# Kernel optimization log

Measured on AMD Instinct MI355X. Metric: run time of the kernel, lower is better.

## Reference

```python
import jax, jax.numpy as jnp
import numpy as np

NODE_LEN = 200000; E = 1000000; BATCH = 128; NT = 2048
IN_FEATS = 256; HID = 128; L1 = 13; L2 = 30; NHEAD = 8; GAMMA = 0.1


def _type_att(xs, W, b, q):
    # xs: [N, T, d] -> [N, d]; type-level (semantic) attention
    s = jnp.einsum('ntd,d->nt', jnp.tanh(xs @ W + b), q)
    a = jax.nn.softmax(s, axis=1)
    return jnp.einsum('nt,ntd->nd', a, xs)


def _add_att(qv, kv, Wq, Wk, v):
    # qv: [N, d], kv: [N, L, d] -> [N, d]; additive attention over L
    t = jnp.tanh((qv @ Wq)[:, None, :] + kv @ Wk)
    a = jax.nn.softmax(jnp.einsum('nld,d->nl', t, v), axis=1)
    return jnp.einsum('nl,nld->nd', a, kv)


def _mha(h, W, b):
    # h: [N, L, D]; W: [4, D, D] (q,k,v,o); b: [4, D]
    N, L, D = h.shape
    hd = D // NHEAD
    def proj(i):
        return (h @ W[i] + b[i]).reshape(N, L, NHEAD, hd).transpose(0, 2, 1, 3)
    q, k, v = proj(0), proj(1), proj(2)
    a = jax.nn.softmax(jnp.einsum('nhld,nhmd->nhlm', q, k) / jnp.sqrt(jnp.float32(hd)), axis=-1)
    o = jnp.einsum('nhlm,nhmd->nhld', a, v).transpose(0, 2, 1, 3).reshape(N, L, D)
    return o @ W[3] + b[3]


def _forward(x, edge_index, batch, rootindex, type_x0, type_x1, type_x2, root1, parent1,
             root2, parent2, type_x3, root3, type_x4, root4, adj,
             W1, b1, W2, b2, mha_W, mha_b, att_Wq, att_Wk, att_v, fuse_W, fuse_b,
             gat_W, gat_a_src, gat_a_dst, ta_W, ta_b, ta_q, gc2_W, gc2_b, fin_W, fin_b):
    n = x.shape[0]
    loop = jnp.arange(n, dtype=edge_index.dtype)
    row = jnp.concatenate([edge_index[0], loop])
    col = jnp.concatenate([edge_index[1], loop])
    deg = jax.ops.segment_sum(jnp.ones(row.shape[0], x.dtype), col, num_segments=n)
    dinv = jax.lax.rsqrt(jnp.maximum(deg, 1.0))
    norm = (dinv[row] * dinv[col])[:, None]

    def gcn(h, W, b):
        m = (h @ W)[row] * norm
        return jax.ops.segment_sum(m, col, num_segments=n) + b

    h1 = gcn(x, W1, b1)                          # conv1
    root_extend = h1[rootindex[batch]]           # per-graph root broadcast (replaces python loop)
    h = jax.nn.relu(jnp.concatenate([h1, root_extend], axis=1))
    h2 = jax.nn.relu(gcn(h, W2, b2))             # conv2
    # sentinel zero row == eye(node_len+1, node_len) one-hot gather semantics
    hp = jnp.concatenate([h2, jnp.zeros((1, h2.shape[1]), h2.dtype)], axis=0)

    x0 = [hp[type_x0]]
    for i, (tx, rid, pid) in enumerate([(type_x1, root1, parent1), (type_x2, root2, parent2)]):
        lst, rt, pr = hp[tx], hp[rid], hp[pid]
        ids = jnp.stack([pr, rt], axis=1)        # [N, 2, d]
        att = _add_att(lst, ids, att_Wq[i], att_Wk[i], att_v[i])
        alpha = jax.nn.sigmoid(jnp.concatenate([lst, att], axis=-1) @ fuse_W[i] + fuse_b[i])[:, None]
        x0.append(alpha * lst + (1.0 - alpha) * att)
    for i, (tx, rid) in enumerate([(type_x3, root3), (type_x4, root4)]):
        seq = _mha(hp[tx], mha_W[i], mha_b[i])   # [N, L, d]
        rt = hp[rid]
        att = _add_att(rt, seq, att_Wq[2 + i], att_Wk[2 + i], att_v[2 + i])
        alpha = jax.nn.sigmoid(jnp.concatenate([rt, att], axis=-1) @ fuse_W[2 + i] + fuse_b[2 + i])[:, None]
        x0.append(alpha * rt + (1.0 - alpha) * att)
    x0.append(hp[type_x0])

    # heterogeneous graph attention conv (gc1) + per-type attention fusion (at1)
    H = jnp.stack([x0[t] @ gat_W[t] for t in range(6)])  # [6, NT, d]
    mask = adj > 0
    x1 = []
    for t1 in range(6):
        msgs = []
        for t2 in range(6):
            e = (H[t1] @ gat_a_src[t1, t2])[:, None] + (H[t2] @ gat_a_dst[t1, t2])[None, :]
            s = jnp.where(mask[t1, t2], jax.nn.leaky_relu(e, negative_slope=GAMMA), -1e9)
            msgs.append(jax.nn.softmax(s, axis=1) @ H[t2])
        m = jnp.stack(msgs, axis=1)                      # [NT, 6, d]
        x1.append(jax.nn.relu(_type_att(m, ta_W[t1], ta_b[t1], ta_q[t1])))
    X1 = jnp.stack(x1)                                   # [6, NT, d]

    # second hop: dense GraphConvolution (gc2) + at2; only type 5 feeds the head
    hx = X1 @ gc2_W
    msgs5 = jnp.einsum('snm,smd->snd', adj[5], hx) + gc2_b
    x2_5 = _type_att(msgs5.transpose(1, 0, 2), ta_W[11], ta_b[11], ta_q[11])
    return jax.nn.log_softmax(x2_5 @ fin_W + fin_b, axis=-1)


def setup_inputs() -> dict:
    key = jax.random.key(0)
    ks = jax.random.split(key, 32)
    f32 = jnp.float32
    x = jax.random.normal(ks[0], (NODE_LEN, IN_FEATS), f32)
    edge_index = jax.random.randint(ks[1], (2, E), 0, NODE_LEN, dtype=jnp.int32)
    batch = jax.random.randint(ks[2], (NODE_LEN,), 0, BATCH, dtype=jnp.int32)
    rootindex = jax.random.randint(ks[3], (BATCH,), 0, NODE_LEN, dtype=jnp.int32)
    idx = lambda k, shape: jax.random.randint(k, shape, 0, NODE_LEN, dtype=jnp.int32)
    type_x0 = idx(ks[4], (NT,)); type_x1 = idx(ks[5], (NT,)); type_x2 = idx(ks[6], (NT,))
    root1 = idx(ks[7], (NT,)); parent1 = idx(ks[8], (NT,))
    root2 = idx(ks[9], (NT,)); parent2 = idx(ks[10], (NT,))
    type_x3 = idx(ks[11], (NT, L1)); root3 = idx(ks[12], (NT,))
    type_x4 = idx(ks[13], (NT, L2)); root4 = idx(ks[14], (NT,))
    adj = (jax.random.uniform(ks[15], (6, 6, NT, NT)) < 0.02).astype(f32)
    p = lambda k, shape: 0.02 * jax.random.normal(k, shape, f32)
    W1 = p(ks[16], (IN_FEATS, HID)); b1 = jnp.zeros((HID,), f32)
    W2 = p(ks[17], (2 * HID, HID)); b2 = jnp.zeros((HID,), f32)
    mha_W = p(ks[18], (2, 4, HID, HID)); mha_b = jnp.zeros((2, 4, HID), f32)
    att_Wq = p(ks[19], (4, HID, HID)); att_Wk = p(ks[20], (4, HID, HID)); att_v = p(ks[21], (4, HID))
    fuse_W = p(ks[22], (4, 2 * HID)); fuse_b = jnp.zeros((4,), f32)
    gat_W = p(ks[23], (6, HID, HID)); gat_a_src = p(ks[24], (6, 6, HID)); gat_a_dst = p(ks[25], (6, 6, HID))
    ta_W = p(ks[26], (12, HID, HID)); ta_b = jnp.zeros((12, HID), f32); ta_q = p(ks[27], (12, HID))
    gc2_W = p(ks[28], (HID, HID)); gc2_b = jnp.zeros((HID,), f32)
    fin_W = p(ks[29], (HID, 4)); fin_b = jnp.zeros((4,), f32)
    return dict(x=x, edge_index=edge_index, batch=batch, rootindex=rootindex,
                type_x0=type_x0, type_x1=type_x1, type_x2=type_x2,
                root1=root1, parent1=parent1, root2=root2, parent2=parent2,
                type_x3=type_x3, root3=root3, type_x4=type_x4, root4=root4, adj=adj,
                W1=W1, b1=b1, W2=W2, b2=b2, mha_W=mha_W, mha_b=mha_b,
                att_Wq=att_Wq, att_Wk=att_Wk, att_v=att_v, fuse_W=fuse_W, fuse_b=fuse_b,
                gat_W=gat_W, gat_a_src=gat_a_src, gat_a_dst=gat_a_dst,
                ta_W=ta_W, ta_b=ta_b, ta_q=ta_q, gc2_W=gc2_W, gc2_b=gc2_b,
                fin_W=fin_W, fin_b=fin_b)


def reference(x, edge_index, batch, rootindex, type_x0, type_x1, type_x2, root1, parent1,
              root2, parent2, type_x3, root3, type_x4, root4, adj,
              W1, b1, W2, b2, mha_W, mha_b, att_Wq, att_Wk, att_v, fuse_W, fuse_b,
              gat_W, gat_a_src, gat_a_dst, ta_W, ta_b, ta_q, gc2_W, gc2_b, fin_W, fin_b):
    return _forward(x, edge_index, batch, rootindex, type_x0, type_x1, type_x2, root1, parent1,
                    root2, parent2, type_x3, root3, type_x4, root4, adj,
                    W1, b1, W2, b2, mha_W, mha_b, att_Wq, att_Wk, att_v, fuse_W, fuse_b,
                    gat_W, gat_a_src, gat_a_dst, ta_W, ta_b, ta_q, gc2_W, gc2_b, fin_W, fin_b)
```

## Files before the change

### kernel.cpp

```cpp
#include <hip/hip_runtime.h>
#include <hip/hip_bf16.h>
#include <math.h>


typedef unsigned short u16;
typedef unsigned int   u32;
typedef __attribute__((ext_vector_type(8))) short short8;
typedef __attribute__((ext_vector_type(4))) float f32x4;

#define NNODE 200000
#define NEDGE 1000000
#define NTT   2048

static constexpr size_t MiB = 1024ull * 1024ull;

enum : unsigned {
    O_W1 = 0,         O_b1 = 32768,     O_W2 = 32896,     O_b2 = 65664,
    O_mhaW = 65792,   O_mhab = 196864,  O_attWq = 197888, O_attWk = 263424,
    O_attv = 328960,  O_fuseW = 329472, O_fuseb = 330496, O_gatW = 330504,
    O_asrc = 428808,  O_adst = 433416,  O_taW = 438024,   O_tab = 634632,
    O_taq = 636168,   O_gc2W = 637704,  O_gc2b = 654088,  O_finW = 654216,
    O_finb = 654728
};

__device__ __forceinline__ float b2f(u16 u) { return __uint_as_float(((u32)u) << 16); }
__device__ __forceinline__ u16 f2b(float f) {
    u32 u = __float_as_uint(f);
    u32 r = (u + 0x7fffu + ((u >> 16) & 1u)) >> 16;
    return (u16)r;
}

__device__ __forceinline__ float wsum(float v) {
#pragma unroll
    for (int m = 1; m < 64; m <<= 1) v += __shfl_xor(v, m, 64);
    return v;
}
__device__ __forceinline__ float bsum128(float v, float* s) {
    v = wsum(v);
    __syncthreads();
    if ((threadIdx.x & 63) == 0) s[threadIdx.x >> 6] = v;
    __syncthreads();
    return s[0] + s[1];
}
__device__ __forceinline__ float bmax128(float v, float* s) {
#pragma unroll
    for (int m = 1; m < 64; m <<= 1) v = fmaxf(v, __shfl_xor(v, m, 64));
    __syncthreads();
    if ((threadIdx.x & 63) == 0) s[threadIdx.x >> 6] = v;
    __syncthreads();
    return fmaxf(s[0], s[1]);
}

__global__ __launch_bounds__(256) void probe_k(const void* xsrc, int* flag) {
    __shared__ int cnt;
    if (threadIdx.x == 0) cnt = 0;
    __syncthreads();
    int c = 0;
    for (int i = threadIdx.x; i < 4096; i += 256) {
        float v = fabsf(b2f(((const u16*)xsrc)[2 * i]));
        if (v > 1e-6f && v < 100.f) c++;
    }
    atomicAdd(&cnt, c);
    __syncthreads();
    if (threadIdx.x == 0) flag[0] = (cnt < 2048) ? 1 : 0;
}

struct CEnt { const void* src; unsigned dstOff; unsigned cnt; };
struct CTab { CEnt e[21]; };
__global__ __launch_bounds__(256) void convp_k(CTab tb, u16* pb, const int* flag) {
    bool f32 = flag[0] != 0;
    int stride = gridDim.x * blockDim.x;
    int tid = blockIdx.x * blockDim.x + threadIdx.x;
    for (int k = 0; k < 21; k++) {
        const void* s = tb.e[k].src;
        unsigned off = tb.e[k].dstOff, n = tb.e[k].cnt;
        for (unsigned i = tid; i < n; i += stride)
            pb[off + i] = f32 ? f2b(((const float*)s)[i]) : ((const u16*)s)[i];
    }
}

template <int K, bool OBF>
__global__ __launch_bounds__(256) void gemm_bf16(const void* __restrict__ A,
                                                 const u16* __restrict__ W,
                                                 const u16* __restrict__ bias,
                                                 void* __restrict__ Cv, int M,
                                                 const int* flagp) {
    constexpr int LW = 40;
    __shared__ u16 Al[128 * LW];
    __shared__ u16 Bl[128 * LW];
    const int tid = threadIdx.x;
    const int lane = tid & 63, wv = tid >> 6;
    const int row0 = blockIdx.x * 128;
    const int m16 = lane & 15, oct = lane >> 4;
    const bool aF32 = flagp && (flagp[0] != 0);

    f32x4 acc[2][8];
#pragma unroll
    for (int s = 0; s < 2; s++)
#pragma unroll
        for (int t = 0; t < 8; t++) acc[s][t] = (f32x4){0.f, 0.f, 0.f, 0.f};

    const int r = tid >> 1, kk16 = (tid & 1) * 16;
    const int gr = row0 + r;
    const bool rowOk = (gr < M);

    for (int k0 = 0; k0 < K; k0 += 32) {
        {
            uint4 d0 = {0, 0, 0, 0}, d1 = {0, 0, 0, 0};
            if (rowOk) {
                if (aF32) {
                    const float* src = (const float*)A + (size_t)gr * K + k0 + kk16;
                    union { uint4 v[2]; u16 u[16]; } t;
#pragma unroll
                    for (int q = 0; q < 16; q++) t.u[q] = f2b(src[q]);
                    d0 = t.v[0];
                    d1 = t.v[1];
                } else {
                    const uint4* src = (const uint4*)((const u16*)A + (size_t)gr * K + k0 + kk16);
                    d0 = src[0];
                    d1 = src[1];
                }
            }
            *(uint4*)&Al[r * LW + kk16] = d0;
            *(uint4*)&Al[r * LW + kk16 + 8] = d1;
        }
#pragma unroll
        for (int ii = 0; ii < 16; ii++) {
            int e = tid + ii * 256;
            int kk = e & 31, n = e >> 5;
            Bl[n * LW + kk] = W[(size_t)(k0 + kk) * 128 + n];
        }
        __syncthreads();

        short8 af0 = *(const short8*)&Al[(wv * 32 + m16) * LW + oct * 8];
        short8 af1 = *(const short8*)&Al[(wv * 32 + 16 + m16) * LW + oct * 8];
        short8 bf[8];
#pragma unroll
        for (int t = 0; t < 8; t++)
            bf[t] = *(const short8*)&Bl[(t * 16 + m16) * LW + oct * 8];
#pragma unroll
        for (int t = 0; t < 8; t++) {
            acc[0][t] = __builtin_amdgcn_mfma_f32_16x16x32_bf16(af0, bf[t], acc[0][t], 0, 0, 0);
            acc[1][t] = __builtin_amdgcn_mfma_f32_16x16x32_bf16(af1, bf[t], acc[1][t], 0, 0, 0);
        }
        __syncthreads();
    }

    float bv[8];
#pragma unroll
    for (int t = 0; t < 8; t++) bv[t] = bias ? b2f(bias[t * 16 + m16]) : 0.f;
#pragma unroll
    for (int s = 0; s < 2; s++)
#pragma unroll
        for (int t = 0; t < 8; t++)
#pragma unroll
            for (int rr = 0; rr < 4; rr++) {
                int orow = row0 + wv * 32 + s * 16 + oct * 4 + rr;
                if (orow < M) {
                    float val = acc[s][t][rr] + bv[t];
                    size_t idx = (size_t)orow * 128 + t * 16 + m16;
                    if (OBF) ((u16*)Cv)[idx] = f2b(val);
                    else     ((float*)Cv)[idx] = val;
                }
            }
}

template <int K, bool OBF>
__global__ __launch_bounds__(256) void gemm_bat_k(const u16* __restrict__ A0, size_t Astride,
                                                  const u16* __restrict__ W0, unsigned Wstride,
                                                  const u16* __restrict__ bias0, unsigned bStride,
                                                  void* __restrict__ Cv, size_t Cstride,
                                                  int M) {
    constexpr int LW = 40;
    __shared__ u16 Al[128 * LW];
    __shared__ u16 Bl[128 * LW];
    const int y = blockIdx.y;
    const u16* A = A0 + (size_t)y * Astride;
    const u16* W = W0 + (size_t)y * Wstride;
    const u16* bias = bias0 ? (bias0 + (size_t)y * bStride) : nullptr;
    const size_t cbase = (size_t)y * Cstride;
    const int tid = threadIdx.x;
    const int lane = tid & 63, wv = tid >> 6;
    const int row0 = blockIdx.x * 128;
    const int m16 = lane & 15, oct = lane >> 4;

    f32x4 acc[2][8];
#pragma unroll
    for (int s = 0; s < 2; s++)
#pragma unroll
        for (int t = 0; t < 8; t++) acc[s][t] = (f32x4){0.f, 0.f, 0.f, 0.f};

    const int r = tid >> 1, kk16 = (tid & 1) * 16;
    const int gr = row0 + r;
    const bool rowOk = (gr < M);

    for (int k0 = 0; k0 < K; k0 += 32) {
        {
            uint4 d0 = {0, 0, 0, 0}, d1 = {0, 0, 0, 0};
            if (rowOk) {
                const uint4* src = (const uint4*)(A + (size_t)gr * K + k0 + kk16);
                d0 = src[0];
                d1 = src[1];
            }
            *(uint4*)&Al[r * LW + kk16] = d0;
            *(uint4*)&Al[r * LW + kk16 + 8] = d1;
        }
#pragma unroll
        for (int ii = 0; ii < 16; ii++) {
            int e = tid + ii * 256;
            int kk = e & 31, n = e >> 5;
            Bl[n * LW + kk] = W[(size_t)(k0 + kk) * 128 + n];
        }
        __syncthreads();

        short8 af0 = *(const short8*)&Al[(wv * 32 + m16) * LW + oct * 8];
        short8 af1 = *(const short8*)&Al[(wv * 32 + 16 + m16) * LW + oct * 8];
        short8 bf[8];
#pragma unroll
        for (int t = 0; t < 8; t++)
            bf[t] = *(const short8*)&Bl[(t * 16 + m16) * LW + oct * 8];
#pragma unroll
        for (int t = 0; t < 8; t++) {
            acc[0][t] = __builtin_amdgcn_mfma_f32_16x16x32_bf16(af0, bf[t], acc[0][t], 0, 0, 0);
            acc[1][t] = __builtin_amdgcn_mfma_f32_16x16x32_bf16(af1, bf[t], acc[1][t], 0, 0, 0);
        }
        __syncthreads();
    }

    float bv[8];
#pragma unroll
    for (int t = 0; t < 8; t++) bv[t] = bias ? b2f(bias[t * 16 + m16]) : 0.f;
#pragma unroll
    for (int s = 0; s < 2; s++)
#pragma unroll
        for (int t = 0; t < 8; t++)
#pragma unroll
            for (int rr = 0; rr < 4; rr++) {
                int orow = row0 + wv * 32 + s * 16 + oct * 4 + rr;
                if (orow < M) {
                    float val = acc[s][t][rr] + bv[t];
                    size_t idx = cbase + (size_t)orow * 128 + t * 16 + m16;
                    if (OBF) ((u16*)Cv)[idx] = f2b(val);
                    else     ((float*)Cv)[idx] = val;
                }
            }
}

__global__ __launch_bounds__(256) void gemm_conv2(const u16* __restrict__ h1r,
                                                  const int* __restrict__ batch,
                                                  const int* __restrict__ rootindex,
                                                  const u16* __restrict__ W,
                                                  u16* __restrict__ C, int M) {
    constexpr int LW = 40;
    __shared__ u16 Al[128 * LW];
    __shared__ u16 Bl[128 * LW];
    const int tid = threadIdx.x;
    const int lane = tid & 63, wv = tid >> 6;
    const int row0 = blockIdx.x * 128;
    const int m16 = lane & 15, oct = lane >> 4;

    f32x4 acc[2][8];
#pragma unroll
    for (int s = 0; s < 2; s++)
#pragma unroll
        for (int t = 0; t < 8; t++) acc[s][t] = (f32x4){0.f, 0.f, 0.f, 0.f};

    const int r = tid >> 1, kk16 = (tid & 1) * 16;
    const int gr = row0 + r;
    const u16* pSelf = nullptr; const u16* pRoot = nullptr;
    if (gr < M) {
        pSelf = h1r + (size_t)gr * 128;
        pRoot = h1r + (size_t)rootindex[batch[gr]] * 128;
    }

    for (int k0 = 0; k0 < 256; k0 += 32) {
        {
            int kg = k0 + kk16;
            uint4 d0 = {0, 0, 0, 0}, d1 = {0, 0, 0, 0};
            if (pSelf) {
                const u16* sp = (kg < 128) ? (pSelf + kg) : (pRoot + kg - 128);
                d0 = ((const uint4*)sp)[0];
                d1 = ((const uint4*)sp)[1];
            }
            *(uint4*)&Al[r * LW + kk16] = d0;
            *(uint4*)&Al[r * LW + kk16 + 8] = d1;
        }
#pragma unroll
        for (int ii = 0; ii < 16; ii++) {
            int e = tid + ii * 256;
            int kk = e & 31, n = e >> 5;
            Bl[n * LW + kk] = W[(size_t)(k0 + kk) * 128 + n];
        }
        __syncthreads();

        short8 af0 = *(const short8*)&Al[(wv * 32 + m16) * LW + oct * 8];
        short8 af1 = *(const short8*)&Al[(wv * 32 + 16 + m16) * LW + oct * 8];
        short8 bf[8];
#pragma unroll
        for (int t = 0; t < 8; t++)
            bf[t] = *(const short8*)&Bl[(t * 16 + m16) * LW + oct * 8];
#pragma unroll
        for (int t = 0; t < 8; t++) {
            acc[0][t] = __builtin_amdgcn_mfma_f32_16x16x32_bf16(af0, bf[t], acc[0][t], 0, 0, 0);
            acc[1][t] = __builtin_amdgcn_mfma_f32_16x16x32_bf16(af1, bf[t], acc[1][t], 0, 0, 0);
        }
        __syncthreads();
    }
#pragma unroll
    for (int s = 0; s < 2; s++)
#pragma unroll
        for (int t = 0; t < 8; t++)
#pragma unroll
            for (int rr = 0; rr < 4; rr++) {
                int orow = row0 + wv * 32 + s * 16 + oct * 4 + rr;
                if (orow < M)
                    C[(size_t)orow * 128 + t * 16 + m16] = f2b(acc[s][t][rr]);
            }
}

__global__ __launch_bounds__(256) void hist_k(const int* __restrict__ ei,
                                              int* __restrict__ cnt) {
    int e = blockIdx.x * 256 + threadIdx.x;
    if (e < NEDGE) atomicAdd(&cnt[ei[NEDGE + e]], 1);
}
__global__ __launch_bounds__(256) void dinv_k(const int* __restrict__ cnt,
                                              float* __restrict__ dinv) {
    int i = blockIdx.x * 256 + threadIdx.x;
    if (i < NNODE) dinv[i] = rsqrtf((float)(cnt[i] + 1));
}
__global__ __launch_bounds__(256) void scan1_k(const int* __restrict__ cnt,
                                               int* __restrict__ bsum) {
    int t = threadIdx.x;
    int base = blockIdx.x * 1024 + t * 4;
    int s = 0;
#pragma unroll
    for (int q = 0; q < 4; q++) {
        int i = base + q;
        if (i < NNODE) s += cnt[i];
    }
#pragma unroll
    for (int m = 1; m < 64; m <<= 1) s += __shfl_xor(s, m, 64);
    __shared__ int ws_[4];
    if ((t & 63) == 0) ws_[t >> 6] = s;
    __syncthreads();
    if (t == 0) bsum[blockIdx.x] = ws_[0] + ws_[1] + ws_[2] + ws_[3];
}
__global__ __launch_bounds__(64) void scan2_k(const int* __restrict__ bsum,
                                              int* __restrict__ bofs, int nb,
                                              int* __restrict__ rowptrN) {
    if (threadIdx.x == 0) {
        int r = 0;
        for (int i = 0; i < nb; i++) { int v = bsum[i]; bofs[i] = r; r += v; }
        *rowptrN = r;
    }
}
__global__ __launch_bounds__(256) void scan3_k(const int* __restrict__ cnt,
                                               const int* __restrict__ bofs,
                                               int* __restrict__ rowptr,
                                               int* __restrict__ cursor) {
    int t = threadIdx.x, lane = t & 63, wv = t >> 6;
    int base = blockIdx.x * 1024 + t * 4;
    int v[4];
    int s = 0;
#pragma unroll
    for (int q = 0; q < 4; q++) {
        int i = base + q;
        v[q] = (i < NNODE) ? cnt[i] : 0;
        s += v[q];
    }
    int inc = s;
#pragma unroll
    for (int d = 1; d < 64; d <<= 1) {
        int u = __shfl_up(inc, d, 64);
        if (lane >= d) inc += u;
    }
    __shared__ int wsum_[4];
    if (lane == 63) wsum_[wv] = inc;
    __syncthreads();
    int wofs = 0;
    for (int w = 0; w < wv; w++) wofs += wsum_[w];
    int ex = bofs[blockIdx.x] + wofs + inc - s;
#pragma unroll
    for (int q = 0; q < 4; q++) {
        int i = base + q;
        if (i < NNODE) { rowptr[i] = ex; cursor[i] = ex; }
        ex += v[q];
    }
}
__global__ __launch_bounds__(256) void fill_k(const int* __restrict__ ei,
                                              int* __restrict__ cursor,
                                              int* __restrict__ csr_src) {
    int e = blockIdx.x * 256 + threadIdx.x;
    if (e < NEDGE) {
        int col = ei[NEDGE + e];
        int pos = atomicAdd(&cursor[col], 1);
        csr_src[pos] = ei[e];
    }
}
template <bool OBF>
__global__ __launch_bounds__(256) void gather_gcn_k(const u16* __restrict__ xwb,
                                                    const int* __restrict__ rowptr,
                                                    const int* __restrict__ csr_src,
                                                    const float* __restrict__ dinv,
                                                    const u16* __restrict__ bias,
                                                    void* __restrict__ out) {
    int node = blockIdx.x * 4 + (threadIdx.x >> 6);
    if (node >= NNODE) return;
    int lane = threadIdx.x & 63;
    int beg = rowptr[node], end = rowptr[node + 1];
    int cnt = end - beg;
    if (cnt < 0) cnt = 0;
    if (cnt > 2048) cnt = 2048;
    end = beg + cnt;
    float di = dinv[node];
    u32 pk = *(const u32*)&xwb[(size_t)node * 128 + lane * 2];
    float selfn = di * di;
    float a0 = b2f((u16)(pk & 0xffffu)) * selfn;
    float a1 = b2f((u16)(pk >> 16)) * selfn;
    int myrow = 0; float mynrm = 0.f;
    if (lane < cnt) {
        myrow = csr_src[beg + lane];
        mynrm = dinv[myrow] * di;
    }
    int n0 = cnt < 64 ? cnt : 64;
    for (int j = 0; j < n0; j++) {
        int row = __shfl(myrow, j, 64);
        float nrm = __shfl(mynrm, j, 64);
        u32 p2 = *(const u32*)&xwb[(size_t)row * 128 + lane * 2];
        a0 += b2f((u16)(p2 & 0xffffu)) * nrm;
        a1 += b2f((u16)(p2 >> 16)) * nrm;
    }
    for (int j = beg + 64; j < end; j++) {
        int row = csr_src[j];
        float nrm = dinv[row] * di;
        u32 p2 = *(const u32*)&xwb[(size_t)row * 128 + lane * 2];
        a0 += b2f((u16)(p2 & 0xffffu)) * nrm;
        a1 += b2f((u16)(p2 >> 16)) * nrm;
    }
// ... 78 lines not shown
        sc[l][m] = s * 0.25f;
    }
    __syncthreads();
    if (t < L) {
        float mx = -3e38f;
        for (int m = 0; m < L; m++) mx = fmaxf(mx, sc[t][m]);
        float z = 0.f;
        for (int m = 0; m < L; m++) { float w = expf(sc[t][m] - mx); sc[t][m] = w; z += w; }
        float izz = 1.f / z;
        for (int m = 0; m < L; m++) sc[t][m] *= izz;
    }
    __syncthreads();
    for (int e = t; e < L * 16; e += 64) {
        int l = e >> 4, d = e & 15;
        float o = 0.f;
        for (int m = 0; m < L; m++) o += sc[l][m] * vs[m][d];
        ao[((size_t)n * L + l) * 128 + h * 16 + d] = f2b(o);
    }
}
__global__ __launch_bounds__(128) void addatt_root_k(const u16* __restrict__ seqo,
                                                     const u16* __restrict__ kpre,
                                                     const float* __restrict__ h2,
                                                     const int* rid,
                                                     const u16* __restrict__ Wq,
                                                     const u16* __restrict__ vv,
                                                     const u16* __restrict__ fw,
                                                     const u16* fbp, int fbi, int L,
                                                     u16* __restrict__ out) {
    int n = blockIdx.x, c = threadIdx.x;
    __shared__ float rt[128], sl[32], red[2];
    rt[c] = h2[(size_t)rid[n] * 128 + c];
    __syncthreads();
    float qc = 0.f;
    for (int k = 0; k < 128; k++) qc += rt[k] * b2f(Wq[k * 128 + c]);
    float vc = b2f(vv[c]);
    for (int l = 0; l < L; l++) {
        float u = qc + b2f(kpre[((size_t)n * L + l) * 128 + c]);
        float s = bsum128(tanhf(u) * vc, red);
        if (c == 0) sl[l] = s;
    }
    __syncthreads();
    float mx = -3e38f;
    for (int l = 0; l < L; l++) mx = fmaxf(mx, sl[l]);
    float z = 0.f;
    for (int l = 0; l < L; l++) z += expf(sl[l] - mx);
    float att = 0.f;
    for (int l = 0; l < L; l++)
        att += expf(sl[l] - mx) * b2f(seqo[((size_t)n * L + l) * 128 + c]);
    att /= z;
    float pa = rt[c] * b2f(fw[c]) + att * b2f(fw[128 + c]);
    float alpha = 1.f / (1.f + expf(-(bsum128(pa, red) + b2f(fbp[fbi]))));
    out[(size_t)n * 128 + c] = f2b(alpha * rt[c] + (1.f - alpha) * att);
}
__global__ __launch_bounds__(128) void gat_e_k(const float* __restrict__ H,
                                               const u16* __restrict__ asrc,
                                               const u16* __restrict__ adst,
                                               float* esrc, float* edst) {
    int p = blockIdx.y, t1 = p / 6, t2 = p % 6;
    int i = blockIdx.x * 128 + threadIdx.x;
    __shared__ float vs[128], vd[128];
    vs[threadIdx.x] = b2f(asrc[p * 128 + threadIdx.x]);
    vd[threadIdx.x] = b2f(adst[p * 128 + threadIdx.x]);
    __syncthreads();
    const float* r1 = H + ((size_t)t1 * NTT + i) * 128;
    const float* r2 = H + ((size_t)t2 * NTT + i) * 128;
    float s1 = 0.f, s2 = 0.f;
    for (int k = 0; k < 128; k++) { s1 += r1[k] * vs[k]; s2 += r2[k] * vd[k]; }
    esrc[p * NTT + i] = s1;
    edst[p * NTT + i] = s2;
}
__global__ __launch_bounds__(128) void gc1_attn_k(const void* __restrict__ adjv,
                                                  const float* __restrict__ H,
                                                  const float* __restrict__ esrc,
                                                  const float* __restrict__ edst,
                                                  u16* __restrict__ msgs,
                                                  const int* flagp) {
    int i = blockIdx.x, p = blockIdx.y, t = threadIdx.x;
    int t2 = p % 6;
    const bool f32 = flagp[0] != 0;
    size_t rowoff = ((size_t)p * NTT + i) * NTT;
    const float* edp = edst + p * NTT;
    float es = esrc[p * NTT + i];
    __shared__ int nzj[2048];
    __shared__ float nzs[2048];
    __shared__ int cnt;
    __shared__ float red[2];
    if (t == 0) cnt = 0;
    __syncthreads();
    int j0 = t * 16;
    float av[16];
    if (f32) {
        const float4* af = (const float4*)((const float*)adjv + rowoff + j0);
#pragma unroll
        for (int q = 0; q < 4; q++) {
            float4 d = af[q];
            av[q * 4 + 0] = d.x; av[q * 4 + 1] = d.y;
            av[q * 4 + 2] = d.z; av[q * 4 + 3] = d.w;
        }
    } else {
        const u16* ab = (const u16*)adjv + rowoff + j0;
        union { uint4 v; u16 u[8]; } a0, a1;
        a0.v = *(const uint4*)(ab);
        a1.v = *(const uint4*)(ab + 8);
#pragma unroll
        for (int q = 0; q < 16; q++) av[q] = b2f(q < 8 ? a0.u[q] : a1.u[q - 8]);
    }
    float lmax = -3e38f;
#pragma unroll
    for (int jj = 0; jj < 16; jj++) {
        if (av[jj] > 0.f) {
            int j = j0 + jj;
            float e = es + edp[j];
            float sv = e > 0.f ? e : 0.1f * e;
            lmax = fmaxf(lmax, sv);
            int kk = atomicAdd(&cnt, 1);
            nzj[kk] = j;
            nzs[kk] = sv;
        }
    }
    float mx = bmax128(lmax, red);
    int nnz = cnt;
    float psum = 0.f;
// ... 34 lines not shown
    float o = 0.f;
    for (int t2 = 0; t2 < 6; t2++)
        o += expf(sv[t2] - mx) * b2f(msgs[(((size_t)t1 * 6 + t2) * NTT + n) * 128 + c]);
    o /= z;
    X1[((size_t)t1 * NTT + n) * 128 + c] = f2b(fmaxf(o, 0.f));
}
__global__ __launch_bounds__(128) void gc2_agg_k(const void* __restrict__ adjv,
                                                 size_t adjBase,
                                                 const float* __restrict__ hx,
                                                 const u16* __restrict__ bias,
                                                 float* __restrict__ msgs5,
                                                 const int* flagp) {
    int i = blockIdx.x, s = blockIdx.y, t = threadIdx.x;
    const bool f32 = flagp[0] != 0;
    size_t rowoff = adjBase + ((size_t)s * NTT + i) * NTT;
    __shared__ int nzj[2048];
    __shared__ float nzw[2048];
    __shared__ int cnt;
    if (t == 0) cnt = 0;
    __syncthreads();
    int j0 = t * 16;
    float av[16];
    if (f32) {
        const float4* af = (const float4*)((const float*)adjv + rowoff + j0);
#pragma unroll
        for (int q = 0; q < 4; q++) {
            float4 d = af[q];
            av[q * 4 + 0] = d.x; av[q * 4 + 1] = d.y;
            av[q * 4 + 2] = d.z; av[q * 4 + 3] = d.w;
        }
    } else {
        const u16* ab = (const u16*)adjv + rowoff + j0;
        union { uint4 v; u16 u[8]; } a0, a1;
        a0.v = *(const uint4*)(ab);
        a1.v = *(const uint4*)(ab + 8);
#pragma unroll
        for (int q = 0; q < 16; q++) av[q] = b2f(q < 8 ? a0.u[q] : a1.u[q - 8]);
    }
#pragma unroll
    for (int jj = 0; jj < 16; jj++) {
        if (av[jj] != 0.f) {
            int kk = atomicAdd(&cnt, 1);
            nzj[kk] = j0 + jj;
            nzw[kk] = av[jj];
        }
    }
    __syncthreads();
    const float* hxs = hx + (size_t)s * NTT * 128;
    float acc = 0.f;
    int nnz = cnt;
    for (int k = 0; k < nnz; k++) acc += nzw[k] * hxs[(size_t)nzj[k] * 128 + t];
    msgs5[((size_t)s * NTT + i) * 128 + t] = acc + b2f(bias[t]);
}
__global__ __launch_bounds__(128) void at2_head_k(const float* __restrict__ msgs5,
                                                  const u16* __restrict__ taW,
                                                  const u16* __restrict__ tab,
                                                  const u16* __restrict__ taq,
                                                  const u16* __restrict__ finW,
                                                  const u16* __restrict__ finb,
                                                  float* __restrict__ out) {
    int n = blockIdx.x, c = threadIdx.x;
    __shared__ float mr[6][128], sv[6], red[2];
    const u16* Wt = taW + (size_t)11 * 16384;
    float bc = b2f(tab[11 * 128 + c]), qcv = b2f(taq[11 * 128 + c]);
    for (int s = 0; s < 6; s++)
        mr[s][c] = msgs5[((size_t)s * NTT + n) * 128 + c];
    __syncthreads();
    for (int s = 0; s < 6; s++) {
        float u = bc;
        for (int k = 0; k < 128; k++) u += mr[s][k] * b2f(Wt[k * 128 + c]);
        float sc = bsum128(tanhf(u) * qcv, red);
        if (c == 0) sv[s] = sc;
    }
    __syncthreads();
    float mx = -3e38f;
    for (int s = 0; s < 6; s++) mx = fmaxf(mx, sv[s]);
    float z = 0.f;
    for (int s = 0; s < 6; s++) z += expf(sv[s] - mx);
    float x2c = 0.f;
    for (int s = 0; s < 6; s++) x2c += expf(sv[s] - mx) * mr[s][c];
    x2c /= z;
    float l0 = bsum128(x2c * b2f(finW[c * 4 + 0]), red) + b2f(finb[0]);
    float l1 = bsum128(x2c * b2f(finW[c * 4 + 1]), red) + b2f(finb[1]);
    float l2 = bsum128(x2c * b2f(finW[c * 4 + 2]), red) + b2f(finb[2]);
    float l3 = bsum128(x2c * b2f(finW[c * 4 + 3]), red) + b2f(finb[3]);
    float m4 = fmaxf(fmaxf(l0, l1), fmaxf(l2, l3));
    float ls = logf(expf(l0 - m4) + expf(l1 - m4) + expf(l2 - m4) + expf(l3 - m4)) + m4;
    if (c < 4) {
        float v = (c == 0) ? l0 : (c == 1) ? l1 : (c == 2) ? l2 : l3;
        out[n * 4 + c] = v - ls;
    }
}

extern "C" void kernel_launch(void* const* d_in, const int* in_sizes, int n_in,
                              void* d_out, int out_size, void* d_ws, size_t ws_size,
                              hipStream_t stream) {
    const void* x       = d_in[0];
    const int* ei       = (const int*)d_in[1];
    const int* batch    = (const int*)d_in[2];
    const int* rootidx  = (const int*)d_in[3];
    const int* type_x0  = (const int*)d_in[4];
    const int* type_x1  = (const int*)d_in[5];
    const int* type_x2  = (const int*)d_in[6];
    const int* root1    = (const int*)d_in[7];
    const int* parent1  = (const int*)d_in[8];
    const int* root2    = (const int*)d_in[9];
    const int* parent2  = (const int*)d_in[10];
    const int* type_x3  = (const int*)d_in[11];
    const int* root3    = (const int*)d_in[12];
    const int* type_x4  = (const int*)d_in[13];
    const int* root4    = (const int*)d_in[14];
    const void* adj     = d_in[15];

    char* ws = (char*)d_ws;
    int*   flag = (int*)(ws);
    u16*   pb   = (u16*)  (ws + 64 * 1024);
    float* dinv = (float*)(ws + 2 * MiB);
    u16*   xwb  = (u16*)  (ws + 3 * MiB);
    float* h2   = (float*)(ws + 52 * MiB);
    u16*   h1r  = (u16*)  (ws + 52 * MiB);
    int*   cnt_i   = (int*)(ws + 150 * MiB);
    int*   rowptr  = (int*)(ws + 151 * MiB);
    int*   cursor  = (int*)(ws + 152 * MiB);
    int*   csr_src = (int*)(ws + 153 * MiB);
    int*   bsum    = (int*)(ws + 158 * MiB);
    int*   bofs    = (int*)(ws + 158 * MiB + 4096);
    u16*   seqb = (u16*)  (ws + 3 * MiB);
    u16*   qb   = (u16*)  (ws + 18 * MiB);
    u16*   kb   = (u16*)  (ws + 33 * MiB);
    u16*   vb   = (u16*)  (ws + 150 * MiB);
    u16*   aob  = (u16*)  (ws + 165 * MiB);
    u16*   seqo = (u16*)  (ws + 18 * MiB);
    u16*   kpre = (u16*)  (ws + 33 * MiB);
    u16*   x0b  = (u16*)  (ws + 180 * MiB);
    u16*   X1b  = (u16*)  (ws + 183 * MiB);
    float* Hb   = (float*)(ws + 52 * MiB);
    float* esrc = (float*)(ws + 58 * MiB);
    float* edst = (float*)(ws + 59 * MiB);
    u16*   msgs = (u16*)  (ws + 60 * MiB);
    u16*   ubuf = (u16*)  (ws + 78 * MiB);
    float* hx   = (float*)(ws + 96 * MiB);
    float* msg5 = (float*)(ws + 102 * MiB);

    probe_k<<<1, 256, 0, stream>>>(x, flag);
    CTab tb;
    int kk = 0;
    auto add = [&](int i, unsigned off, unsigned n) {
        tb.e[kk].src = d_in[i]; tb.e[kk].dstOff = off; tb.e[kk].cnt = n; kk++;
    };
    add(16, O_W1, 32768);   add(17, O_b1, 128);     add(18, O_W2, 32768);
    add(19, O_b2, 128);     add(20, O_mhaW, 131072);add(21, O_mhab, 1024);
    add(22, O_attWq, 65536);add(23, O_attWk, 65536);add(24, O_attv, 512);
    add(25, O_fuseW, 1024); add(26, O_fuseb, 4);    add(27, O_gatW, 98304);
    add(28, O_asrc, 4608);  add(29, O_adst, 4608);  add(30, O_taW, 196608);
    add(31, O_tab, 1536);   add(32, O_taq, 1536);   add(33, O_gc2W, 16384);
    add(34, O_gc2b, 128);   add(35, O_finW, 512);   add(36, O_finb, 4);
    convp_k<<<256, 256, 0, stream>>>(tb, pb, flag);

    const int NB = (NNODE + 1023) / 1024;
    hipMemsetAsync(cnt_i, 0, (size_t)NNODE * 4, stream);
    hist_k<<<(NEDGE + 255) / 256, 256, 0, stream>>>(ei, cnt_i);
    dinv_k<<<(NNODE + 255) / 256, 256, 0, stream>>>(cnt_i, dinv);
    scan1_k<<<NB, 256, 0, stream>>>(cnt_i, bsum);
    scan2_k<<<1, 64, 0, stream>>>(bsum, bofs, NB, rowptr + NNODE);
    scan3_k<<<NB, 256, 0, stream>>>(cnt_i, bofs, rowptr, cursor);
    fill_k<<<(NEDGE + 255) / 256, 256, 0, stream>>>(ei, cursor, csr_src);

    gemm_bf16<256, true><<<(NNODE + 127) / 128, 256, 0, stream>>>(x, pb + O_W1, (const u16*)nullptr, xwb, NNODE, flag);
    gather_gcn_k<true><<<(NNODE + 3) / 4, 256, 0, stream>>>(xwb, rowptr, csr_src, dinv, pb + O_b1, h1r);

    gemm_conv2<<<(NNODE + 127) / 128, 256, 0, stream>>>(h1r, batch, rootidx, pb + O_W2, xwb, NNODE);
    gather_gcn_k<false><<<(NNODE + 3) / 4, 256, 0, stream>>>(xwb, rowptr, csr_src, dinv, pb + O_b2, h2);

    x0copy_k<<<(NTT * 128) / 256, 256, 0, stream>>>(h2, type_x0, x0b);
    addatt12_k<<<NTT, 128, 0, stream>>>(h2, type_x1, root1, parent1,
                                        pb + O_attWq, pb + O_attWk, pb + O_attv,
                                        pb + O_fuseW, pb + O_fuseb, 0,
                                        x0b + 1 * NTT * 128);
    addatt12_k<<<NTT, 128, 0, stream>>>(h2, type_x2, root2, parent2,
                                        pb + O_attWq + 16384, pb + O_attWk + 16384,
                                        pb + O_attv + 128, pb + O_fuseW + 256,
                                        pb + O_fuseb, 1,
                                        x0b + 2 * NTT * 128);
    for (int i = 0; i < 2; i++) {
        int L = i ? 30 : 13;
        const int* tx = i ? type_x4 : type_x3;
        const int* rt = i ? root4 : root3;
        int M = NTT * L;
        gather_seq_k<<<(M * 128 + 255) / 256, 256, 0, stream>>>(h2, tx, seqb, M * 128);
        gemm_bf16<128, true><<<(M + 127) / 128, 256, 0, stream>>>(seqb, pb + O_mhaW + (i * 4 + 0) * 16384,
                                                                  pb + O_mhab + (i * 4 + 0) * 128, qb, M, nullptr);
        gemm_bf16<128, true><<<(M + 127) / 128, 256, 0, stream>>>(seqb, pb + O_mhaW + (i * 4 + 1) * 16384,
                                                                  pb + O_mhab + (i * 4 + 1) * 128, kb, M, nullptr);
        gemm_bf16<128, true><<<(M + 127) / 128, 256, 0, stream>>>(seqb, pb + O_mhaW + (i * 4 + 2) * 16384,
                                                                  pb + O_mhab + (i * 4 + 2) * 128, vb, M, nullptr);
        mha_attn_k<<<dim3(NTT, 8), 64, 0, stream>>>(qb, kb, vb, aob, L);
        gemm_bf16<128, true><<<(M + 127) / 128, 256, 0, stream>>>(aob, pb + O_mhaW + (i * 4 + 3) * 16384,
                                                                  pb + O_mhab + (i * 4 + 3) * 128, seqo, M, nullptr);
        gemm_bf16<128, true><<<(M + 127) / 128, 256, 0, stream>>>(seqo, pb + O_attWk + (2 + i) * 16384,
                                                                  (const u16*)nullptr, kpre, M, nullptr);
        addatt_root_k<<<NTT, 128, 0, stream>>>(seqo, kpre, h2, rt,
                                               pb + O_attWq + (2 + i) * 16384,
                                               pb + O_attv + (2 + i) * 128,
                                               pb + O_fuseW + (2 + i) * 256,
                                               pb + O_fuseb, 2 + i, L,
                                               x0b + (3 + i) * NTT * 128);
    }

    gemm_bat_k<128, false><<<dim3(NTT / 128, 6), 256, 0, stream>>>(
        x0b, (size_t)NTT * 128, pb + O_gatW, 16384, (const u16*)nullptr, 0,
        Hb, (size_t)NTT * 128, NTT);
    gat_e_k<<<dim3(16, 36), 128, 0, stream>>>(Hb, pb + O_asrc, pb + O_adst, esrc, edst);
    gc1_attn_k<<<dim3(NTT, 36), 128, 0, stream>>>(adj, Hb, esrc, edst, msgs, flag);
    gemm_bat_k<128, true><<<dim3((6 * NTT) / 128, 6), 256, 0, stream>>>(
        msgs, (size_t)6 * NTT * 128, pb + O_taW, 16384, pb + O_tab, 128,
        ubuf, (size_t)6 * NTT * 128, 6 * NTT);
    at1_lite_k<<<dim3(NTT, 6), 128, 0, stream>>>(msgs, ubuf, pb + O_taq, X1b);
    gemm_bf16<128, false><<<(6 * NTT) / 128, 256, 0, stream>>>(X1b, pb + O_gc2W, (const u16*)nullptr, hx, 6 * NTT, nullptr);
    gc2_agg_k<<<dim3(NTT, 6), 128, 0, stream>>>(adj, (size_t)5 * 6 * NTT * NTT, hx,
                                                pb + O_gc2b, msg5, flag);
    at2_head_k<<<NTT, 128, 0, stream>>>(msg5, pb + O_taW, pb + O_tab, pb + O_taq,
                                        pb + O_finW, pb + O_finb, (float*)d_out);
}
```

Before: 2.266 ms.

## Pre-transpose GEMM weights, vectorize loads, move final type-attention projection to MFMA GEMM

Weights are transposed once during parameter conversion so every GEMM loads its B tile with two 16-byte vector loads per thread instead of 16 strided scalar loads. The f32 A path now uses float4 loads. The dinv kernel is folded into scan3, and gat_e is reworked so four threads share a row with vectorized loads. The final head's per-thread scalar 128x128 matvec is replaced by an MFMA GEMM into a bf16 buffer, which adds a launch plus an intermediate write and read, and rounds that projection output to bf16.

```diff
diff --git a/kernel.cpp b/kernel.cpp
--- a/kernel.cpp
+++ b/kernel.cpp
@@ -22,6 +22,10 @@
     O_taq = 636168,   O_gc2W = 637704,  O_gc2b = 654088,  O_finW = 654216,
     O_finb = 654728
 };
+enum : unsigned {
+    T_W1 = 0,          T_W2 = 32768,     T_mhaW = 65536,   T_attWk = 196608,
+    T_gatW = 262144,   T_taW = 360448,   T_gc2W = 557056
+};
 
 __device__ __forceinline__ float b2f(u16 u) { return __uint_as_float(((u32)u) << 16); }
 __device__ __forceinline__ u16 f2b(float f) {
@@ -62,12 +66,18 @@
     }
     atomicAdd(&cnt, c);
     __syncthreads();
-    if (threadIdx.x == 0) flag[0] = (cnt < 2048) ? 1 : 0;
+    if (threadIdx.x == 0) {
+        flag[0] = (cnt < 2048) ? 1 : 0;
+        flag[1] = 1;
+    }
 }
 
 struct CEnt { const void* src; unsigned dstOff; unsigned cnt; };
 struct CTab { CEnt e[21]; };
-__global__ __launch_bounds__(256) void convp_k(CTab tb, u16* pb, const int* flag) {
+struct TEnt { const void* src; unsigned dstOff; unsigned cnt; int msh; int ksh; };
+struct TTab { TEnt e[7]; };
+__global__ __launch_bounds__(256) void convp_k(CTab tb, TTab tt, u16* pb, u16* pbT,
+                                               const int* flag) {
     bool f32 = flag[0] != 0;
     int stride = gridDim.x * blockDim.x;
     int tid = blockIdx.x * blockDim.x + threadIdx.x;
@@ -77,11 +87,22 @@
         for (unsigned i = tid; i < n; i += stride)
             pb[off + i] = f32 ? f2b(((const float*)s)[i]) : ((const u16*)s)[i];
     }
+    for (int k = 0; k < 7; k++) {
+        const void* s = tt.e[k].src;
+        unsigned off = tt.e[k].dstOff, n = tt.e[k].cnt;
+        int msh = tt.e[k].msh, ksh = tt.e[k].ksh;
+        for (unsigned i = tid; i < n; i += stride) {
+            unsigned mat = i >> msh, r = i & ((1u << msh) - 1);
+            unsigned kk = r >> 7, nn = r & 127;
+            unsigned dst = (mat << msh) + (nn << ksh) + kk;
+            pbT[off + dst] = f32 ? f2b(((const float*)s)[i]) : ((const u16*)s)[i];
+        }
+    }
 }
 
 template <int K, bool OBF>
 __global__ __launch_bounds__(256) void gemm_bf16(const void* __restrict__ A,
-                                                 const u16* __restrict__ W,
+                                                 const u16* __restrict__ WT,
                                                  const u16* __restrict__ bias,
                                                  void* __restrict__ Cv, int M,
                                                  const int* flagp) {
@@ -109,10 +130,14 @@
             uint4 d0 = {0, 0, 0, 0}, d1 = {0, 0, 0, 0};
             if (rowOk) {
                 if (aF32) {
-                    const float* src = (const float*)A + (size_t)gr * K + k0 + kk16;
+                    const float4* s4 = (const float4*)((const float*)A + (size_t)gr * K + k0 + kk16);
                     union { uint4 v[2]; u16 u[16]; } t;
 #pragma unroll
-                    for (int q = 0; q < 16; q++) t.u[q] = f2b(src[q]);
+                    for (int q = 0; q < 4; q++) {
+                        float4 f = s4[q];
+                        t.u[q * 4 + 0] = f2b(f.x); t.u[q * 4 + 1] = f2b(f.y);
+                        t.u[q * 4 + 2] = f2b(f.z); t.u[q * 4 + 3] = f2b(f.w);
+                    }
                     d0 = t.v[0];
                     d1 = t.v[1];
                 } else {
@@ -124,11 +149,10 @@
             *(uint4*)&Al[r * LW + kk16] = d0;
             *(uint4*)&Al[r * LW + kk16 + 8] = d1;
         }
-#pragma unroll
-        for (int ii = 0; ii < 16; ii++) {
-            int e = tid + ii * 256;
-            int kk = e & 31, n = e >> 5;
-            Bl[n * LW + kk] = W[(size_t)(k0 + kk) * 128 + n];
+        {
+            const uint4* wsrc = (const uint4*)(WT + (size_t)r * K + k0 + kk16);
+            *(uint4*)&Bl[r * LW + kk16] = wsrc[0];
+            *(uint4*)&Bl[r * LW + kk16 + 8] = wsrc[1];
         }
         __syncthreads();
 
@@ -176,7 +200,7 @@
     __shared__ u16 Bl[128 * LW];
     const int y = blockIdx.y;
     const u16* A = A0 + (size_t)y * Astride;
-    const u16* W = W0 + (size_t)y * Wstride;
+    const u16* WT = W0 + (size_t)y * Wstride;
     const u16* bias = bias0 ? (bias0 + (size_t)y * bStride) : nullptr;
     const size_t cbase = (size_t)y * Cstride;
     const int tid = threadIdx.x;
@@ -205,11 +229,10 @@
             *(uint4*)&Al[r * LW + kk16] = d0;
             *(uint4*)&Al[r * LW + kk16 + 8] = d1;
         }
-#pragma unroll
-        for (int ii = 0; ii < 16; ii++) {
-            int e = tid + ii * 256;
-            int kk = e & 31, n = e >> 5;
-            Bl[n * LW + kk] = W[(size_t)(k0 + kk) * 128 + n];
+        {
+            const uint4* wsrc = (const uint4*)(WT + (size_t)r * K + k0 + kk16);
+            *(uint4*)&Bl[r * LW + kk16] = wsrc[0];
+            *(uint4*)&Bl[r * LW + kk16 + 8] = wsrc[1];
         }
         __syncthreads();
 
@@ -249,7 +272,7 @@
 __global__ __launch_bounds__(256) void gemm_conv2(const u16* __restrict__ h1r,
                                                   const int* __restrict__ batch,
                                                   const int* __restrict__ rootindex,
-                                                  const u16* __restrict__ W,
+                                                  const u16* __restrict__ WT,
                                                   u16* __restrict__ C, int M) {
     constexpr int LW = 40;
     __shared__ u16 Al[128 * LW];
@@ -285,11 +308,10 @@
             *(uint4*)&Al[r * LW + kk16] = d0;
             *(uint4*)&Al[r * LW + kk16 + 8] = d1;
         }
-#pragma unroll
-        for (int ii = 0; ii < 16; ii++) {
-            int e = tid + ii * 256;
-            int kk = e & 31, n = e >> 5;
-            Bl[n * LW + kk] = W[(size_t)(k0 + kk) * 128 + n];
+        {
+            const uint4* wsrc = (const uint4*)(WT + (size_t)r * 256 + k0 + kk16);
+            *(uint4*)&Bl[r * LW + kk16] = wsrc[0];
+            *(uint4*)&Bl[r * LW + kk16 + 8] = wsrc[1];
         }
         __syncthreads();
 
@@ -322,11 +344,6 @@
                                               int* __restrict__ cnt) {
     int e = blockIdx.x * 256 + threadIdx.x;
     if (e < NEDGE) atomicAdd(&cnt[ei[NEDGE + e]], 1);
-}
-__global__ __launch_bounds__(256) void dinv_k(const int* __restrict__ cnt,
-                                              float* __restrict__ dinv) {
-    int i = blockIdx.x * 256 + threadIdx.x;
-    if (i < NNODE) dinv[i] = rsqrtf((float)(cnt[i] + 1));
 }
 __global__ __launch_bounds__(256) void scan1_k(const int* __restrict__ cnt,
                                                int* __restrict__ bsum) {
@@ -357,7 +374,8 @@
 __global__ __launch_bounds__(256) void scan3_k(const int* __restrict__ cnt,
                                                const int* __restrict__ bofs,
                                                int* __restrict__ rowptr,
-                                               int* __restrict__ cursor) {
+                                               int* __restrict__ cursor,
+                                               float* __restrict__ dinv) {
     int t = threadIdx.x, lane = t & 63, wv = t >> 6;
     int base = blockIdx.x * 1024 + t * 4;
     int v[4];
@@ -383,7 +401,11 @@
 #pragma unroll
     for (int q = 0; q < 4; q++) {
         int i = base + q;
-        if (i < NNODE) { rowptr[i] = ex; cursor[i] = ex; }
+        if (i < NNODE) {
+            rowptr[i] = ex;
+            cursor[i] = ex;
+            dinv[i] = rsqrtf((float)(v[q] + 1));
+        }
         ex += v[q];
     }
 }
@@ -568,22 +590,34 @@
     float alpha = 1.f / (1.f + expf(-(bsum128(pa, red) + b2f(fbp[fbi]))));
     out[(size_t)n * 128 + c] = f2b(alpha * rt[c] + (1.f - alpha) * att);
 }
-__global__ __launch_bounds__(128) void gat_e_k(const float* __restrict__ H,
-                                               const u16* __restrict__ asrc,
-                                               const u16* __restrict__ adst,
-                                               float* esrc, float* edst) {
+__global__ __launch_bounds__(128) void gat_e2_k(const float* __restrict__ H,
+                                                const u16* __restrict__ asrc,
+                                                const u16* __restrict__ adst,
+                                                float* esrc, float* edst) {
     int p = blockIdx.y, t1 = p / 6, t2 = p % 6;
-    int i = blockIdx.x * 128 + threadIdx.x;
+    int t = threadIdx.x;
     __shared__ float vs[128], vd[128];
-    vs[threadIdx.x] = b2f(asrc[p * 128 + threadIdx.x]);
-    vd[threadIdx.x] = b2f(adst[p * 128 + threadIdx.x]);
-    __syncthreads();
-    const float* r1 = H + ((size_t)t1 * NTT + i) * 128;
-    const float* r2 = H + ((size_t)t2 * NTT + i) * 128;
+    vs[t] = b2f(asrc[p * 128 + t]);
+    vd[t] = b2f(adst[p * 128 + t]);
+    __syncthreads();
+    int row = t >> 2, part = t & 3;
+    int i = blockIdx.x * 32 + row;
+    const float4* r1 = (const float4*)(H + ((size_t)t1 * NTT + i) * 128 + part * 32);
+    const float4* r2 = (const float4*)(H + ((size_t)t2 * NTT + i) * 128 + part * 32);
     float s1 = 0.f, s2 = 0.f;
-    for (int k = 0; k < 128; k++) { s1 += r1[k] * vs[k]; s2 += r2[k] * vd[k]; }
-    esrc[p * NTT + i] = s1;
-    edst[p * NTT + i] = s2;
+#pragma unroll
+    for (int q = 0; q < 8; q++) {
+        float4 a = r1[q], b = r2[q];
+        int kb = part * 32 + q * 4;
+        s1 += a.x * vs[kb] + a.y * vs[kb + 1] + a.z * vs[kb + 2] + a.w * vs[kb + 3];
+        s2 += b.x * vd[kb] + b.y * vd[kb + 1] + b.z * vd[kb + 2] + b.w * vd[kb + 3];
+    }
+    s1 += __shfl_xor(s1, 1, 64); s1 += __shfl_xor(s1, 2, 64);
+    s2 += __shfl_xor(s2, 1, 64); s2 += __shfl_xor(s2, 2, 64);
+    if (part == 0) {
+        esrc[p * NTT + i] = s1;
+        edst[p * NTT + i] = s2;
+    }
 }
 __global__ __launch_bounds__(128) void gc1_attn_k(const void* __restrict__ adjv,
                                                   const float* __restrict__ H,
@@ -724,23 +758,17 @@
     for (int k = 0; k < nnz; k++) acc += nzw[k] * hxs[(size_t)nzj[k] * 128 + t];
     msgs5[((size_t)s * NTT + i) * 128 + t] = acc + b2f(bias[t]);
 }
-__global__ __launch_bounds__(128) void at2_head_k(const float* __restrict__ msgs5,
-                                                  const u16* __restrict__ taW,
-                                                  const u16* __restrict__ tab,
-                                                  const u16* __restrict__ taq,
-                                                  const u16* __restrict__ finW,
-                                                  const u16* __restrict__ finb,
-                                                  float* __restrict__ out) {
+__global__ __launch_bounds__(128) void at2_head_lite_k(const float* __restrict__ msgs5,
+                                                       const u16* __restrict__ ubuf2,
+                                                       const u16* __restrict__ taq,
+                                                       const u16* __restrict__ finW,
+                                                       const u16* __restrict__ finb,
+                                                       float* __restrict__ out) {
     int n = blockIdx.x, c = threadIdx.x;
-    __shared__ float mr[6][128], sv[6], red[2];
-    const u16* Wt = taW + (size_t)11 * 16384;
-    float bc = b2f(tab[11 * 128 + c]), qcv = b2f(taq[11 * 128 + c]);
-    for (int s = 0; s < 6; s++)
-        mr[s][c] = msgs5[((size_t)s * NTT + n) * 128 + c];
-    __syncthreads();
+    __shared__ float sv[6], red[2];
+    float qcv = b2f(taq[11 * 128 + c]);
     for (int s = 0; s < 6; s++) {
-        float u = bc;
-        for (int k = 0; k < 128; k++) u += mr[s][k] * b2f(Wt[k * 128 + c]);
+        float u = b2f(ubuf2[((size_t)s * NTT + n) * 128 + c]);
         float sc = bsum128(tanhf(u) * qcv, red);
         if (c == 0) sv[s] = sc;
     }
@@ -750,7 +778,8 @@
     float z = 0.f;
     for (int s = 0; s < 6; s++) z += expf(sv[s] - mx);
     float x2c = 0.f;
-    for (int s = 0; s < 6; s++) x2c += expf(sv[s] - mx) * mr[s][c];
+    for (int s = 0; s < 6; s++)
+        x2c += expf(sv[s] - mx) * msgs5[((size_t)s * NTT + n) * 128 + c];
     x2c /= z;
     float l0 = bsum128(x2c * b2f(finW[c * 4 + 0]), red) + b2f(finb[0]);
     float l1 = bsum128(x2c * b2f(finW[c * 4 + 1]), red) + b2f(finb[1]);
@@ -813,6 +842,8 @@
     u16*   ubuf = (u16*)  (ws + 78 * MiB);
     float* hx   = (float*)(ws + 96 * MiB);
     float* msg5 = (float*)(ws + 102 * MiB);
+    u16*   ubuf2= (u16*)  (ws + 60 * MiB);
+    u16*   pbT  = (u16*)  (ws + 186 * MiB);
 
     probe_k<<<1, 256, 0, stream>>>(x, flag);
     CTab tb;
@@ -827,21 +858,33 @@
     add(28, O_asrc, 4608);  add(29, O_adst, 4608);  add(30, O_taW, 196608);
     add(31, O_tab, 1536);   add(32, O_taq, 1536);   add(33, O_gc2W, 16384);
     add(34, O_gc2b, 128);   add(35, O_finW, 512);   add(36, O_finb, 4);
-    convp_k<<<256, 256, 0, stream>>>(tb, pb, flag);
+    TTab tt;
+    int tk = 0;
+    auto addt = [&](int i, unsigned off, unsigned n, int msh, int ksh) {
+        tt.e[tk].src = d_in[i]; tt.e[tk].dstOff = off; tt.e[tk].cnt = n;
+        tt.e[tk].msh = msh; tt.e[tk].ksh = ksh; tk++;
+    };
+    addt(16, T_W1, 32768, 15, 8);
+    addt(18, T_W2, 32768, 15, 8);
+    addt(20, T_mhaW, 131072, 14, 7);
+    addt(23, T_attWk, 65536, 14, 7);
+    addt(27, T_gatW, 98304, 14, 7);
+    addt(30, T_taW, 196608, 14, 7);
+    addt(33, T_gc2W, 16384, 14, 7);
+    convp_k<<<256, 256, 0, stream>>>(tb, tt, pb, pbT, flag);
 
     const int NB = (NNODE + 1023) / 1024;
     hipMemsetAsync(cnt_i, 0, (size_t)NNODE * 4, stream);
     hist_k<<<(NEDGE + 255) / 256, 256, 0, stream>>>(ei, cnt_i);
-    dinv_k<<<(NNODE + 255) / 256, 256, 0, stream>>>(cnt_i, dinv);
     scan1_k<<<NB, 256, 0, stream>>>(cnt_i, bsum);
     scan2_k<<<1, 64, 0, stream>>>(bsum, bofs, NB, rowptr + NNODE);
-    scan3_k<<<NB, 256, 0, stream>>>(cnt_i, bofs, rowptr, cursor);
+    scan3_k<<<NB, 256, 0, stream>>>(cnt_i, bofs, rowptr, cursor, dinv);
     fill_k<<<(NEDGE + 255) / 256, 256, 0, stream>>>(ei, cursor, csr_src);
 
-    gemm_bf16<256, true><<<(NNODE + 127) / 128, 256, 0, stream>>>(x, pb + O_W1, (const u16*)nullptr, xwb, NNODE, flag);
+    gemm_bf16<256, true><<<(NNODE + 127) / 128, 256, 0, stream>>>(x, pbT + T_W1, (const u16*)nullptr, xwb, NNODE, flag);
     gather_gcn_k<true><<<(NNODE + 3) / 4, 256, 0, stream>>>(xwb, rowptr, csr_src, dinv, pb + O_b1, h1r);
 
-    gemm_conv2<<<(NNODE + 127) / 128, 256, 0, stream>>>(h1r, batch, rootidx, pb + O_W2, xwb, NNODE);
+    gemm_conv2<<<(NNODE + 127) / 128, 256, 0, stream>>>(h1r, batch, rootidx, pbT + T_W2, xwb, NNODE);
     gather_gcn_k<false><<<(NNODE + 3) / 4, 256, 0, stream>>>(xwb, rowptr, csr_src, dinv, pb + O_b2, h2);
 
     x0copy_k<<<(NTT * 128) / 256, 256, 0, stream>>>(h2, type_x0, x0b);
@@ -860,16 +903,16 @@
         const int* rt = i ? root4 : root3;
         int M = NTT * L;
         gather_seq_k<<<(M * 128 + 255) / 256, 256, 0, stream>>>(h2, tx, seqb, M * 128);
-        gemm_bf16<128, true><<<(M + 127) / 128, 256, 0, stream>>>(seqb, pb + O_mhaW + (i * 4 + 0) * 16384,
+        gemm_bf16<128, true><<<(M + 127) / 128, 256, 0, stream>>>(seqb, pbT + T_mhaW + (i * 4 + 0) * 16384,
                                                                   pb + O_mhab + (i * 4 + 0) * 128, qb, M, nullptr);
-        gemm_bf16<128, true><<<(M + 127) / 128, 256, 0, stream>>>(seqb, pb + O_mhaW + (i * 4 + 1) * 16384,
+        gemm_bf16<128, true><<<(M + 127) / 128, 256, 0, stream>>>(seqb, pbT + T_mhaW + (i * 4 + 1) * 16384,
                                                                   pb + O_mhab + (i * 4 + 1) * 128, kb, M, nullptr);
-        gemm_bf16<128, true><<<(M + 127) / 128, 256, 0, stream>>>(seqb, pb + O_mhaW + (i * 4 + 2) * 16384,
+        gemm_bf16<128, true><<<(M + 127) / 128, 256, 0, stream>>>(seqb, pbT + T_mhaW + (i * 4 + 2) * 16384,
                                                                   pb + O_mhab + (i * 4 + 2) * 128, vb, M, nullptr);
         mha_attn_k<<<dim3(NTT, 8), 64, 0, stream>>>(qb, kb, vb, aob, L);
-        gemm_bf16<128, true><<<(M + 127) / 128, 256, 0, stream>>>(aob, pb + O_mhaW + (i * 4 + 3) * 16384,
+        gemm_bf16<128, true><<<(M + 127) / 128, 256, 0, stream>>>(aob, pbT + T_mhaW + (i * 4 + 3) * 16384,
                                                                   pb + O_mhab + (i * 4 + 3) * 128, seqo, M, nullptr);
-        gemm_bf16<128, true><<<(M + 127) / 128, 256, 0, stream>>>(seqo, pb + O_attWk + (2 + i) * 16384,
+        gemm_bf16<128, true><<<(M + 127) / 128, 256, 0, stream>>>(seqo, pbT + T_attWk + (2 + i) * 16384,
                                                                   (const u16*)nullptr, kpre, M, nullptr);
         addatt_root_k<<<NTT, 128, 0, stream>>>(seqo, kpre, h2, rt,
                                                pb + O_attWq + (2 + i) * 16384,
@@ -880,17 +923,19 @@
     }
 
     gemm_bat_k<128, false><<<dim3(NTT / 128, 6), 256, 0, stream>>>(
-        x0b, (size_t)NTT * 128, pb + O_gatW, 16384, (const u16*)nullptr, 0,
+        x0b, (size_t)NTT * 128, pbT + T_gatW, 16384, (const u16*)nullptr, 0,
         Hb, (size_t)NTT * 128, NTT);
-    gat_e_k<<<dim3(16, 36), 128, 0, stream>>>(Hb, pb + O_asrc, pb + O_adst, esrc, edst);
+    gat_e2_k<<<dim3(NTT / 32, 36), 128, 0, stream>>>(Hb, pb + O_asrc, pb + O_adst, esrc, edst);
     gc1_attn_k<<<dim3(NTT, 36), 128, 0, stream>>>(adj, Hb, esrc, edst, msgs, flag);
     gemm_bat_k<128, true><<<dim3((6 * NTT) / 128, 6), 256, 0, stream>>>(
-        msgs, (size_t)6 * NTT * 128, pb + O_taW, 16384, pb + O_tab, 128,
+        msgs, (size_t)6 * NTT * 128, pbT + T_taW, 16384, pb + O_tab, 128,
         ubuf, (size_t)6 * NTT * 128, 6 * NTT);
     at1_lite_k<<<dim3(NTT, 6), 128, 0, stream>>>(msgs, ubuf, pb + O_taq, X1b);
-    gemm_bf16<128, false><<<(6 * NTT) / 128, 256, 0, stream>>>(X1b, pb + O_gc2W, (const u16*)nullptr, hx, 6 * NTT, nullptr);
+    gemm_bf16<128, false><<<(6 * NTT) / 128, 256, 0, stream>>>(X1b, pbT + T_gc2W, (const u16*)nullptr, hx, 6 * NTT, nullptr);
     gc2_agg_k<<<dim3(NTT, 6), 128, 0, stream>>>(adj, (size_t)5 * 6 * NTT * NTT, hx,
                                                 pb + O_gc2b, msg5, flag);
-    at2_head_k<<<NTT, 128, 0, stream>>>(msg5, pb + O_taW, pb + O_tab, pb + O_taq,
-                                        pb + O_finW, pb + O_finb, (float*)d_out);
-}
+    gemm_bf16<128, true><<<(6 * NTT) / 128, 256, 0, stream>>>(msg5, pbT + T_taW + 11 * 16384,
+                                                              pb + O_tab + 11 * 128, ubuf2, 6 * NTT, flag + 1);
+    at2_head_lite_k<<<NTT, 128, 0, stream>>>(msg5, ubuf2, pb + O_taq,
+                                             pb + O_finW, pb + O_finb, (float*)d_out);
+}
```

After: 2.001 ms. 1.13x faster.
